# Kernel tuning notes

Hardware: AMD Instinct MI355X
Metric: run time of the kernel (lower is better)

The kernel has to match this reference:

```python
import jax, jax.numpy as jnp
import numpy as np

SIZE = 896      # GRU hidden size
HALF = SIZE // 2
BINS = 256      # 2**(bits/2), bits=16
B, T = 16, 1000


def _scale(t):
    # [0, BINS-1] ints -> [-1, 1] floats
    return t.astype(jnp.float32) / ((BINS - 1) / 2.0) - 1.0


def setup_inputs() -> dict:
    key = jax.random.key(0)
    ks = jax.random.split(key, 13)
    s = 0.05
    return {
        "conditional": jax.random.normal(ks[0], (B, T, 3, SIZE), jnp.float32),
        "gru_input_bias": jax.random.normal(ks[1], (3 * SIZE,), jnp.float32) * s,
        "W_h": jax.random.normal(ks[2], (3 * SIZE, SIZE), jnp.float32) * s,   # project_hidden
        "b_h": jax.random.normal(ks[3], (3 * SIZE,), jnp.float32) * s,
        "W_ci": jax.random.normal(ks[4], (3 * HALF, 2), jnp.float32) * s,     # project_coarse_input
        "b_ci": jax.random.normal(ks[5], (3 * HALF,), jnp.float32) * s,
        "W_fi": jax.random.normal(ks[6], (3 * HALF, 3), jnp.float32) * s,     # project_fine_input
        "b_fi": jax.random.normal(ks[7], (3 * HALF,), jnp.float32) * s,
        "W_bc": jax.random.normal(ks[8], (BINS, HALF), jnp.float32) * s,      # to_bins_coarse
        "b_bc": jax.random.normal(ks[9], (BINS,), jnp.float32) * s,
        "W_bf": jax.random.normal(ks[10], (BINS, HALF), jnp.float32) * s,     # to_bins_fine
        "b_bf": jax.random.normal(ks[11], (BINS,), jnp.float32) * s,
    }


def reference(conditional, gru_input_bias, W_h, b_h, W_ci, b_ci, W_fi, b_fi,
              W_bc, b_bc, W_bf, b_bf):
    # Fold input-GRU biases into the conditional (as the torch code does in-place)
    cond = conditional + gru_input_bias.reshape(3, SIZE)  # [B,T,3,SIZE]
    # split each gate into coarse/fine halves and regroup as (r,u,e)
    cc = jnp.concatenate([cond[:, :, 0, :HALF], cond[:, :, 1, :HALF], cond[:, :, 2, :HALF]], -1)
    cf = jnp.concatenate([cond[:, :, 0, HALF:], cond[:, :, 1, HALF:], cond[:, :, 2, HALF:]], -1)
    cc = jnp.transpose(cc, (1, 0, 2))  # [T,B,3*HALF]
    cf = jnp.transpose(cf, (1, 0, 2))
    sample_key = jax.random.key(1)

    # initial state: split_signal(0) -> coarse=fine=0 -> scaled to -1
    init = (-jnp.ones((B, 1), jnp.float32), -jnp.ones((B, 1), jnp.float32),
            jnp.zeros((B, HALF), jnp.float32), jnp.zeros((B, HALF), jnp.float32))

    def step(carry, xs):
        cv, fv, ch, fh = carry
        ccond, fcond, t = xs
        k1, k2 = jax.random.split(jax.random.fold_in(sample_key, t))
        hidden = jnp.concatenate([ch, fh], 1)                   # [B,SIZE]
        hp = hidden @ W_h.T + b_h                               # [B,3*SIZE]
        hcr, hfr, hcu, hfu, hce, hfe = jnp.split(hp, 6, axis=1)
        h_cru = jnp.concatenate([hcr, hcu], 1)
        h_fru = jnp.concatenate([hfr, hfu], 1)
        # coarse half-step
        cin = jnp.concatenate([cv, fv], 1)                      # [B,2]
        cp = cin @ W_ci.T + b_ci + ccond                        # [B,3*HALF]
        ru = jax.nn.sigmoid(cp[:, :SIZE] + h_cru)
        r, u = jnp.split(ru, 2, axis=1)
        e = jnp.tanh(r * hce + cp[:, SIZE:])
        ch = u * ch + (1.0 - u) * e
        logits_c = ch @ W_bc.T + b_bc                           # [B,BINS]
        sc = jax.random.categorical(k1, jax.nn.log_softmax(logits_c, axis=1))
        cv = _scale(sc)[:, None]
        # fine half-step
        fin = jnp.concatenate([cin, cv], 1)                     # [B,3]
        fp = fin @ W_fi.T + b_fi + fcond
        ru = jax.nn.sigmoid(fp[:, :SIZE] + h_fru)
        r, u = jnp.split(ru, 2, axis=1)
        e = jnp.tanh(r * hfe + fp[:, SIZE:])
        fh = u * fh + (1.0 - u) * e
        logits_f = fh @ W_bf.T + b_bf
        sf = jax.random.categorical(k2, jax.nn.log_softmax(logits_f, axis=1))
        fv = _scale(sf)[:, None]
        return (cv, fv, ch, fh), (sc, sf)

    (cv, fv, ch, fh), (oc, of) = jax.lax.scan(step, init, (cc, cf, jnp.arange(T)))
    hidden = jnp.concatenate([ch, fh], 1)
    return oc.T, of.T, hidden  # [B,T] int, [B,T] int, [B,SIZE]
```

## Files before the change

kernel.cpp:

```cpp
#include <hip/hip_runtime.h>
#include <stdint.h>

#define BB 16
#define TT 1000
#define SZ 896
#define HF 448
#define NC 112
#define NWG 240
#define LDS_FLOATS 30112
#define LDS_BYTES (LDS_FLOATS * 4)

typedef float f32x4 __attribute__((ext_vector_type(4)));
typedef float f32x2 __attribute__((ext_vector_type(2)));

__device__ float g_hid[2 * BB * SZ];
__device__ float g_hpc4[BB * HF * 4];
__device__ float g_hpf4[BB * HF * 4];
__device__ uint32_t g_cdone[NC * 16];
__device__ uint32_t g_chrdy[BB * 16];
__device__ uint32_t g_fhrdy[BB * 16];
__device__ unsigned long long g_afl[BB * 4 * 8];
__device__ unsigned long long g_bfl[BB * 4 * 8];

__device__ __forceinline__ void cload4x4(const float* p, f32x4& a0, f32x4& a1, f32x4& a2, f32x4& a3) {
  asm volatile(
      "global_load_dwordx4 %0, %4, off sc0 sc1\n\t"
      "global_load_dwordx4 %1, %4, off offset:16 sc0 sc1\n\t"
      "global_load_dwordx4 %2, %4, off offset:32 sc0 sc1\n\t"
      "global_load_dwordx4 %3, %4, off offset:48 sc0 sc1\n\t"
      "s_waitcnt vmcnt(0)"
      : "=&v"(a0), "=&v"(a1), "=&v"(a2), "=&v"(a3) : "v"(p) : "memory");
}
__device__ __forceinline__ f32x4 cload1x4(const float* p) {
  f32x4 a;
  asm volatile("global_load_dwordx4 %0, %1, off sc0 sc1\n\ts_waitcnt vmcnt(0)"
               : "=&v"(a) : "v"(p) : "memory");
  return a;
}
__device__ __forceinline__ void cstore4d(float* p, f32x4 v) {
  asm volatile("global_store_dwordx4 %0, %1, off sc0 sc1\n\ts_waitcnt vmcnt(0)"
               :: "v"(p), "v"(v) : "memory");
}
__device__ __forceinline__ void cstore1u_nw(uint32_t* p, uint32_t v) {
  asm volatile("global_store_dword %0, %1, off sc0 sc1" :: "v"(p), "v"(v) : "memory");
}
__device__ __forceinline__ void cstore2u_nw(unsigned long long* p, f32x2 v) {
  asm volatile("global_store_dwordx2 %0, %1, off sc0 sc1" :: "v"(p), "v"(v) : "memory");
}

__device__ __forceinline__ void waitFlag(uint32_t* f, uint32_t target) {
  while (__hip_atomic_load(f, __ATOMIC_RELAXED, __HIP_MEMORY_SCOPE_AGENT) < target)
    __builtin_amdgcn_s_sleep(1);
}
__device__ __forceinline__ void waitFlagA(uint32_t* f, uint32_t target) {
  while (__hip_atomic_load(f, __ATOMIC_RELAXED, __HIP_MEMORY_SCOPE_AGENT) < target)
    __builtin_amdgcn_s_sleep(2);
}
__device__ __forceinline__ unsigned long long waitFlag64(unsigned long long* f, uint32_t tag) {
  unsigned long long u;
  while ((uint32_t)((u = __hip_atomic_load(f, __ATOMIC_RELAXED, __HIP_MEMORY_SCOPE_AGENT)) >> 48) < tag)
    __builtin_amdgcn_s_sleep(1);
  return u;
}

__device__ __forceinline__ uint32_t rotl32(uint32_t v, int d) {
  return (v << d) | (v >> (32 - d));
}

__device__ __forceinline__ uint2 tf2(uint32_t k0, uint32_t k1, uint32_t x0, uint32_t x1) {
  const uint32_t k2 = k0 ^ k1 ^ 0x1BD11BDAu;
  x0 += k0; x1 += k1;
  x0 += x1; x1 = rotl32(x1,13); x1 ^= x0;
  x0 += x1; x1 = rotl32(x1,15); x1 ^= x0;
  x0 += x1; x1 = rotl32(x1,26); x1 ^= x0;
  x0 += x1; x1 = rotl32(x1, 6); x1 ^= x0;
  x0 += k1; x1 += k2 + 1u;
  x0 += x1; x1 = rotl32(x1,17); x1 ^= x0;
  x0 += x1; x1 = rotl32(x1,29); x1 ^= x0;
  x0 += x1; x1 = rotl32(x1,16); x1 ^= x0;
  x0 += x1; x1 = rotl32(x1,24); x1 ^= x0;
  x0 += k2; x1 += k0 + 2u;
  x0 += x1; x1 = rotl32(x1,13); x1 ^= x0;
  x0 += x1; x1 = rotl32(x1,15); x1 ^= x0;
  x0 += x1; x1 = rotl32(x1,26); x1 ^= x0;
  x0 += x1; x1 = rotl32(x1, 6); x1 ^= x0;
  x0 += k0; x1 += k1 + 3u;
  x0 += x1; x1 = rotl32(x1,17); x1 ^= x0;
  x0 += x1; x1 = rotl32(x1,29); x1 ^= x0;
  x0 += x1; x1 = rotl32(x1,16); x1 ^= x0;
  x0 += x1; x1 = rotl32(x1,24); x1 ^= x0;
  x0 += k1; x1 += k2 + 4u;
  x0 += x1; x1 = rotl32(x1,13); x1 ^= x0;
  x0 += x1; x1 = rotl32(x1,15); x1 ^= x0;
  x0 += x1; x1 = rotl32(x1,26); x1 ^= x0;
  x0 += x1; x1 = rotl32(x1, 6); x1 ^= x0;
  x0 += k2; x1 += k0 + 5u;
  return make_uint2(x0, x1);
}

__device__ __forceinline__ float gumbel_bits(uint32_t bits) {
  const float tiny = 1.17549435e-38f;
  float f = __uint_as_float((bits >> 9) | 0x3f800000u) - 1.0f;
  float u = fmaxf(tiny, f + tiny);
  return -logf(-logf(u));
}

__device__ __forceinline__ void logits64(const float* __restrict__ wlds,
                                         const float* __restrict__ vec,
                                         float* __restrict__ plds, int tid) {
  const int w = tid >> 6, lane = tid & 63;
  float a = 0.f;
  const float* wp = wlds + (56 * w) * 65 + lane;
  const float* cp = vec + 56 * w;
#pragma unroll 8
  for (int ii = 0; ii < 56; ++ii)
    a = fmaf(cp[ii], wp[ii * 65], a);
  plds[(w << 6) | lane] = a;
}

__global__ __launch_bounds__(256, 1) void wavernn_init() {
  const int idx = blockIdx.x * 256 + threadIdx.x;
  g_hid[idx] = 0.f;
  if (idx < NC * 16) g_cdone[idx] = 0u;
  if (idx < BB * 16) { g_chrdy[idx] = 0u; g_fhrdy[idx] = 0u; }
  if (idx < BB * 4 * 8) { g_afl[idx] = 0ull; g_bfl[idx] = 0ull; }
}

__global__ __launch_bounds__(512, 1) void wavernn_main(
    const float* __restrict__ cond, const float* __restrict__ gib,
    const float* __restrict__ W_h,  const float* __restrict__ b_h,
    const float* __restrict__ W_ci, const float* __restrict__ b_ci,
    const float* __restrict__ W_fi, const float* __restrict__ b_fi,
    const float* __restrict__ W_bc, const float* __restrict__ b_bc,
    const float* __restrict__ W_bf, const float* __restrict__ b_bf,
    float* __restrict__ out) {
  extern __shared__ float smem[];
  const int wg = blockIdx.x, tid = threadIdx.x;

  if (wg < NC) {
    float* hlds = smem;
    const int wave = tid >> 6, lane = tid & 63;
    const int l32 = lane >> 1, b2 = lane & 1;
    const int tp = wave >> 2;
    const int chan = (wg << 2) | (wave & 3);
    const int rb = tp ? (HF + chan) : chan;
    float4 w[3][7];
    float brow[3];
#pragma unroll
    for (int r = 0; r < 3; ++r) {
      const int row = r * SZ + rb;
      brow[r] = b_h[row];
#pragma unroll
      for (int m = 0; m < 7; ++m)
        w[r][m] = *(const float4*)&W_h[(size_t)row * SZ + 4 * l32 + 128 * m];
    }
    const int r16 = tid & 15, c28 = tid >> 4;

    for (int t = 0; t < TT; ++t) {
      const int p = (t & 1) ^ 1;
      if (tid < BB) waitFlagA(&g_chrdy[tid * 16], (uint32_t)t);
      __syncthreads();
      if (c28 < 28) {
        const float* src = g_hid + (size_t)p * BB * SZ + r16 * SZ + c28 * 16;
        f32x4 a0, a1, a2, a3;
        cload4x4(src, a0, a1, a2, a3);
        float* dst = hlds + r16 * 900 + c28 * 16;
        *(f32x4*)(dst) = a0; *(f32x4*)(dst + 4) = a1;
        *(f32x4*)(dst + 8) = a2; *(f32x4*)(dst + 12) = a3;
      }
      __syncthreads();
      float acc[3][8];
#pragma unroll
      for (int r = 0; r < 3; ++r)
#pragma unroll
        for (int i = 0; i < 8; ++i) acc[r][i] = 0.f;
#pragma unroll
      for (int i = 0; i < 8; ++i) {
        const int b = b2 + 2 * i;
        const float* hb = hlds + b * 900 + 4 * l32;
        const float4 h0 = *(const float4*)(hb);
        const float4 h1 = *(const float4*)(hb + 128);
        const float4 h2 = *(const float4*)(hb + 256);
#pragma unroll
        for (int r = 0; r < 3; ++r) {
          float s = acc[r][i];
          s = fmaf(w[r][0].x, h0.x, s); s = fmaf(w[r][0].y, h0.y, s);
          s = fmaf(w[r][0].z, h0.z, s); s = fmaf(w[r][0].w, h0.w, s);
          s = fmaf(w[r][1].x, h1.x, s); s = fmaf(w[r][1].y, h1.y, s);
          s = fmaf(w[r][1].z, h1.z, s); s = fmaf(w[r][1].w, h1.w, s);
          s = fmaf(w[r][2].x, h2.x, s); s = fmaf(w[r][2].y, h2.y, s);
          s = fmaf(w[r][2].z, h2.z, s); s = fmaf(w[r][2].w, h2.w, s);
          acc[r][i] = s;
        }
        if (l32 < 16) {
          const float4 h3 = *(const float4*)(hb + 384);
#pragma unroll
          for (int r = 0; r < 3; ++r) {
            float s = acc[r][i];
            s = fmaf(w[r][3].x, h3.x, s); s = fmaf(w[r][3].y, h3.y, s);
            s = fmaf(w[r][3].z, h3.z, s); s = fmaf(w[r][3].w, h3.w, s);
            acc[r][i] = s;
          }
        }
      }
      if (tid < BB) waitFlag(&g_fhrdy[tid * 16], (uint32_t)t);
      __syncthreads();
      if (c28 < 28) {
        const float* src = g_hid + (size_t)p * BB * SZ + r16 * SZ + HF + c28 * 16;
        f32x4 a0, a1, a2, a3;
        cload4x4(src, a0, a1, a2, a3);
        float* dst = hlds + r16 * 900 + HF + c28 * 16;
        *(f32x4*)(dst) = a0; *(f32x4*)(dst + 4) = a1;
        *(f32x4*)(dst + 8) = a2; *(f32x4*)(dst + 12) = a3;
      }
      __syncthreads();
#pragma unroll
      for (int i = 0; i < 8; ++i) {
        const int b = b2 + 2 * i;
        const float* hb = hlds + b * 900 + 4 * l32;
        if (l32 >= 16) {
          const float4 h3 = *(const float4*)(hb + 384);
#pragma unroll
          for (int r = 0; r < 3; ++r) {
            float s = acc[r][i];
            s = fmaf(w[r][3].x, h3.x, s); s = fmaf(w[r][3].y, h3.y, s);
            s = fmaf(w[r][3].z, h3.z, s); s = fmaf(w[r][3].w, h3.w, s);
            acc[r][i] = s;
          }
        }
        const float4 h4 = *(const float4*)(hb + 512);
        const float4 h5 = *(const float4*)(hb + 640);
        const float4 h6 = *(const float4*)(hb + 768);
#pragma unroll
        for (int r = 0; r < 3; ++r) {
          float s = acc[r][i];
          s = fmaf(w[r][4].x, h4.x, s); s = fmaf(w[r][4].y, h4.y, s);
          s = fmaf(w[r][4].z, h4.z, s); s = fmaf(w[r][4].w, h4.w, s);
          s = fmaf(w[r][5].x, h5.x, s); s = fmaf(w[r][5].y, h5.y, s);
          s = fmaf(w[r][5].z, h5.z, s); s = fmaf(w[r][5].w, h5.w, s);
          s = fmaf(w[r][6].x, h6.x, s); s = fmaf(w[r][6].y, h6.y, s);
          s = fmaf(w[r][6].z, h6.z, s); s = fmaf(w[r][6].w, h6.w, s);
          acc[r][i] = s;
        }
      }
#pragma unroll
      for (int r = 0; r < 3; ++r)
#pragma unroll
        for (int i = 0; i < 8; ++i) {
          float v = acc[r][i];
          v += __shfl_xor(v, 2);
          v += __shfl_xor(v, 4);
          v += __shfl_xor(v, 8);
          v += __shfl_xor(v, 16);
          v += __shfl_xor(v, 32);
          acc[r][i] = v;
        }
      if (lane < 16) {
        const int bb = lane, i = lane >> 1;
        f32x4 hv;
        hv.x = acc[0][i] + brow[0];
        hv.y = acc[1][i] + brow[1];
        hv.z = acc[2][i] + brow[2];
        hv.w = 0.f;
        float* dst = (tp ? g_hpf4 : g_hpc4) + ((size_t)bb * HF + chan) * 4;
        cstore4d(dst, hv);
      }
      __syncthreads();
      if (tid == 0) cstore1u_nw(&g_cdone[wg * 16], (uint32_t)(t + 1));
    }
  } else {
    const int swg = wg - NC;
    const int b = swg >> 3;
    const int role = (swg >> 2) & 1;
    const int k = swg & 3;
    float* wlds = smem;
    float* vlds = smem + 29120;
    float* plds = smem + 29568;
    float* aS = smem + 30080;
    int*   aI = (int*)(smem + 30084);
    float* bS = smem + 30088;
    int*   bI = (int*)(smem + 30092);
    {
      const float* Wm = role ? W_bf : W_bc;
      for (int i = tid; i < HF * 64; i += 512) {
        const int bn = i / HF, kk = i - bn * HF;
        wlds[kk * 65 + bn] = Wm[(size_t)(64 * k + bn) * HF + kk];
      }
    }
    const float* bias = role ? b_bf : b_bc;
    float gw0[3], gw1[3], gw2[3], gbe[3], pc[3];
    if (tid < HF) {
      if (role == 0) {
#pragma unroll
        for (int g = 0; g < 3; ++g) {
          const int rr = g * HF + tid;
          gw0[g] = W_ci[2 * rr]; gw1[g] = W_ci[2 * rr + 1]; gw2[g] = 0.f;
          gbe[g] = b_ci[rr] + gib[g * SZ + tid];
          pc[g] = cond[(((size_t)b * TT) * 3 + g) * SZ + tid];
        }
      } else {
#pragma unroll
        for (int g = 0; g < 3; ++g) {
          const int rr = g * HF + tid;
          gw0[g] = W_fi[3 * rr]; gw1[g] = W_fi[3 * rr + 1]; gw2[g] = W_fi[3 * rr + 2];
          gbe[g] = b_fi[rr] + gib[g * SZ + HF + tid];
          pc[g] = cond[(((size_t)b * TT) * 3 + g) * SZ + HF + tid];
        }
      }
      vlds[tid] = 0.f;
    }
    __syncthreads();
    float cvO = -1.f;
    float fvO = -1.f;

    for (int t = 0; t < TT; ++t) {
      const int q = t & 1;
      const uint2 kf = tf2(0u, 1u, 0u, (uint32_t)t);
      float gub = 0.f;
      if (tid < 64) {
        const uint2 kk = role ? tf2(kf.x, kf.y, 0u, 1u) : tf2(kf.x, kf.y, 0u, 0u);
        const uint2 o = tf2(kk.x, kk.y, 0u, (uint32_t)(b * 256 + 64 * k + tid));
        gub = gumbel_bits(o.x ^ o.y);
      }
      if (role == 0) {
        if (t > 0 && tid >= 452 && tid < 456) {
          const unsigned long long u = waitFlag64(&g_bfl[(b * 4 + (tid - 452)) * 8], (uint32_t)t);
          bS[tid - 452] = __uint_as_float((uint32_t)u);
          bI[tid - 452] = (int)((u >> 40) & 255u);
        }
        if (tid < NC) waitFlag(&g_cdone[tid * 16], (uint32_t)(t + 1));
        __syncthreads();
        float fvv = -1.f;
        if (t > 0) {
          float ms = bS[0]; int sf = bI[0];
#pragma unroll
          for (int m = 1; m < 4; ++m) {
            const float so = bS[m]; const int io = bI[m];
            if (so > ms || (so == ms && io < sf)) { ms = so; sf = io; }
          }
          fvv = (float)sf / 127.5f - 1.0f;
        }
        if (tid < HF) {
          const f32x4 hp = cload1x4(&g_hpc4[((size_t)b * HF + tid) * 4]);
          const float cp0 = fmaf(cvO, gw0[0], fmaf(fvv, gw1[0], gbe[0])) + pc[0];
          const float cp1 = fmaf(cvO, gw0[1], fmaf(fvv, gw1[1], gbe[1])) + pc[1];
          const float cp2 = fmaf(cvO, gw0[2], fmaf(fvv, gw1[2], gbe[2])) + pc[2];
          const float rg = 1.f / (1.f + expf(-(cp0 + hp.x)));
          const float ug = 1.f / (1.f + expf(-(cp1 + hp.y)));
          const float eg = tanhf(fmaf(rg, hp.z, cp2));
          vlds[tid] = ug * vlds[tid] + (1.f - ug) * eg;
        }
        __syncthreads();
        if (k == 0) {
          if (tid < 112)
            cstore4d(&g_hid[(size_t)q * BB * SZ + b * SZ + 4 * tid], *(f32x4*)&vlds[4 * tid]);
          __syncthreads();
          if (tid == 0) cstore1u_nw(&g_chrdy[b * 16], (uint32_t)(t + 1));
        }
        logits64(wlds, vlds, plds, tid);
        __syncthreads();
        if (tid < 64) {
          const float p0 = plds[tid],       p1 = plds[64 + tid];
          const float p2 = plds[128 + tid], p3 = plds[192 + tid];
          const float p4 = plds[256 + tid], p5 = plds[320 + tid];
          const float p6 = plds[384 + tid], p7 = plds[448 + tid];
          const float sum = ((p0 + p1) + (p2 + p3)) + ((p4 + p5) + (p6 + p7));
          float s = (sum + bias[64 * k + tid]) + gub;
          int idx = 64 * k + tid;
#pragma unroll
          for (int m = 1; m < 64; m <<= 1) {
            const float so = __shfl_xor(s, m);
            const int io = __shfl_xor(idx, m);
            if (so > s || (so == s && io < idx)) { s = so; idx = io; }
          }
          if (tid == 0) {
            f32x2 v; v.x = s;
            v.y = __uint_as_float(((uint32_t)(t + 1) << 16) | ((uint32_t)idx << 8));
            cstore2u_nw(&g_afl[(b * 4 + k) * 8], v);
          }
        }
        if (tid >= 448 && tid < 452) {
          const unsigned long long u = waitFlag64(&g_afl[(b * 4 + (tid - 448)) * 8], (uint32_t)(t + 1));
          aS[tid - 448] = __uint_as_float((uint32_t)u);
          aI[tid - 448] = (int)((u >> 40) & 255u);
        }
        __syncthreads();
        {
          float ms = aS[0]; int sc = aI[0];
#pragma unroll
          for (int m = 1; m < 4; ++m) {
            const float so = aS[m]; const int io = aI[m];
            if (so > ms || (so == ms && io < sc)) { ms = so; sc = io; }
          }
          cvO = (float)sc / 127.5f - 1.0f;
          if (k == 0 && tid == 0) out[b * TT + t] = (float)sc;
        }
        if (tid < HF && t + 1 < TT) {
#pragma unroll
          for (int g = 0; g < 3; ++g)
            pc[g] = cond[(((size_t)b * TT + (t + 1)) * 3 + g) * SZ + tid];
        }
      } else {
        if (tid < NC) waitFlag(&g_cdone[tid * 16], (uint32_t)(t + 1));
        __syncthreads();
        f32x4 hp = {0.f, 0.f, 0.f, 0.f};
        if (tid < HF) hp = cload1x4(&g_hpf4[((size_t)b * HF + tid) * 4]);
        if (tid >= 448 && tid < 452) {
          const unsigned long long u = waitFlag64(&g_afl[(b * 4 + (tid - 448)) * 8], (uint32_t)(t + 1));
          aS[tid - 448] = __uint_as_float((uint32_t)u);
          aI[tid - 448] = (int)((u >> 40) & 255u);
        }
        __syncthreads();
        float ms = aS[0]; int sc = aI[0];
#pragma unroll
        for (int m = 1; m < 4; ++m) {
          const float so = aS[m]; const int io = aI[m];
          if (so > ms || (so == ms && io < sc)) { ms = so; sc = io; }
        }
        const float cvNew = (float)sc / 127.5f - 1.0f;
        if (tid < HF) {
          const float fp0 = fmaf(cvO, gw0[0], fmaf(fvO, gw1[0], fmaf(cvNew, gw2[0], gbe[0]))) + pc[0];
          const float fp1 = fmaf(cvO, gw0[1], fmaf(fvO, gw1[1], fmaf(cvNew, gw2[1], gbe[1]))) + pc[1];
          const float fp2 = fmaf(cvO, gw0[2], fmaf(fvO, gw1[2], fmaf(cvNew, gw2[2], gbe[2]))) + pc[2];
          const float rg = 1.f / (1.f + expf(-(fp0 + hp.x)));
          const float ug = 1.f / (1.f + expf(-(fp1 + hp.y)));
          const float eg = tanhf(fmaf(rg, hp.z, fp2));
          vlds[tid] = ug * vlds[tid] + (1.f - ug) * eg;
        }
        __syncthreads();
        if (k == 0) {
          if (tid < 112)
            cstore4d(&g_hid[(size_t)q * BB * SZ + b * SZ + HF + 4 * tid], *(f32x4*)&vlds[4 * tid]);
          __syncthreads();
          if (tid == 0) cstore1u_nw(&g_fhrdy[b * 16], (uint32_t)(t + 1));
        }
        logits64(wlds, vlds, plds, tid);
        __syncthreads();
        if (tid < 64) {
          const float p0 = plds[tid],       p1 = plds[64 + tid];
          const float p2 = plds[128 + tid], p3 = plds[192 + tid];
          const float p4 = plds[256 + tid], p5 = plds[320 + tid];
          const float p6 = plds[384 + tid], p7 = plds[448 + tid];
          const float sum = ((p0 + p1) + (p2 + p3)) + ((p4 + p5) + (p6 + p7));
          float s = (sum + bias[64 * k + tid]) + gub;
          int idx = 64 * k + tid;
#pragma unroll
          for (int m = 1; m < 64; m <<= 1) {
            const float so = __shfl_xor(s, m);
            const int io = __shfl_xor(idx, m);
            if (so > s || (so == s && io < idx)) { s = so; idx = io; }
          }
          if (tid == 0) {
            f32x2 v; v.x = s;
            v.y = __uint_as_float(((uint32_t)(t + 1) << 16) | ((uint32_t)idx << 8));
            cstore2u_nw(&g_bfl[(b * 4 + k) * 8], v);
          }
        }
        if (tid >= 448 && tid < 452) {
          const unsigned long long u = waitFlag64(&g_bfl[(b * 4 + (tid - 448)) * 8], (uint32_t)(t + 1));
          bS[tid - 448] = __uint_as_float((uint32_t)u);
          bI[tid - 448] = (int)((u >> 40) & 255u);
        }
        __syncthreads();
        {
          float msf = bS[0]; int sf = bI[0];
#pragma unroll
          for (int m = 1; m < 4; ++m) {
            const float so = bS[m]; const int io = bI[m];
            if (so > msf || (so == msf && io < sf)) { msf = so; sf = io; }
          }
          fvO = (float)sf / 127.5f - 1.0f;
          if (k == 0 && tid == 0) out[BB * TT + b * TT + t] = (float)sf;
        }
        cvO = cvNew;
        if (tid < HF && t + 1 < TT) {
#pragma unroll
          for (int g = 0; g < 3; ++g)
            pc[g] = cond[(((size_t)b * TT + (t + 1)) * 3 + g) * SZ + HF + tid];
        }
      }
    }
    if (k == 0 && tid < HF) {
      if (role == 0) out[2 * BB * TT + (size_t)b * SZ + tid] = vlds[tid];
      else           out[2 * BB * TT + (size_t)b * SZ + HF + tid] = vlds[tid];
    }
  }
}

extern "C" void kernel_launch(void* const* d_in, const int* in_sizes, int n_in,
                              void* d_out, int out_size, void* d_ws, size_t ws_size,
                              hipStream_t stream) {
  (void)in_sizes; (void)n_in; (void)out_size; (void)d_ws; (void)ws_size;
  const float* cond = (const float*)d_in[0];
  const float* gib  = (const float*)d_in[1];
  const float* W_h  = (const float*)d_in[2];
  const float* b_h  = (const float*)d_in[3];
  const float* W_ci = (const float*)d_in[4];
  const float* b_ci = (const float*)d_in[5];
  const float* W_fi = (const float*)d_in[6];
  const float* b_fi = (const float*)d_in[7];
  const float* W_bc = (const float*)d_in[8];
  const float* b_bc = (const float*)d_in[9];
  const float* W_bf = (const float*)d_in[10];
  const float* b_bf = (const float*)d_in[11];
  float* out = (float*)d_out;
  hipFuncSetAttribute((const void*)wavernn_main,
                      hipFuncAttributeMaxDynamicSharedMemorySize, LDS_BYTES);
  wavernn_init<<<NC, 256, 0, stream>>>();
  wavernn_main<<<NWG, 512, LDS_BYTES, stream>>>(cond, gib, W_h, b_h, W_ci, b_ci,
                                                W_fi, b_fi, W_bc, b_bc, W_bf, b_bf, out);
}
```

Measured before the change: 13.01 ms.

## Replace separate ready flags with step tags embedded alongside each data value

Each hidden-state and projection value is now stored next to a float timestep tag. Consumers poll the data itself until every tag reaches the expected step, instead of waiting on separate counter flags. This removes the store-wait-barrier-then-flag round trips and the extra flag polls on the inter-workgroup critical path, and every one of the four k-workgroups now publishes its own slice. In exchange the exchanged buffers double in size and the spin loops reload wider data, and it relies on 8-byte pairs being written atomically.

```diff
diff --git a/kernel.cpp b/kernel.cpp
--- a/kernel.cpp
+++ b/kernel.cpp
@@ -13,48 +13,44 @@
 typedef float f32x4 __attribute__((ext_vector_type(4)));
 typedef float f32x2 __attribute__((ext_vector_type(2)));
 
-__device__ float g_hid[2 * BB * SZ];
-__device__ float g_hpc4[BB * HF * 4];
-__device__ float g_hpf4[BB * HF * 4];
-__device__ uint32_t g_cdone[NC * 16];
-__device__ uint32_t g_chrdy[BB * 16];
-__device__ uint32_t g_fhrdy[BB * 16];
+__device__ float g_hc[BB * HF * 2];
+__device__ float g_hf[BB * HF * 2];
+__device__ float g_hpc[BB * HF * 8];
+__device__ float g_hpf[BB * HF * 8];
 __device__ unsigned long long g_afl[BB * 4 * 8];
 __device__ unsigned long long g_bfl[BB * 4 * 8];
 
-__device__ __forceinline__ void cload4x4(const float* p, f32x4& a0, f32x4& a1, f32x4& a2, f32x4& a3) {
+#define au(x) __float_as_uint(x)
+
+__device__ __forceinline__ void cload7x4(const float* p, f32x4& a0, f32x4& a1, f32x4& a2,
+                                         f32x4& a3, f32x4& a4, f32x4& a5, f32x4& a6) {
   asm volatile(
-      "global_load_dwordx4 %0, %4, off sc0 sc1\n\t"
-      "global_load_dwordx4 %1, %4, off offset:16 sc0 sc1\n\t"
-      "global_load_dwordx4 %2, %4, off offset:32 sc0 sc1\n\t"
-      "global_load_dwordx4 %3, %4, off offset:48 sc0 sc1\n\t"
+      "global_load_dwordx4 %0, %7, off sc0 sc1\n\t"
+      "global_load_dwordx4 %1, %7, off offset:16 sc0 sc1\n\t"
+      "global_load_dwordx4 %2, %7, off offset:32 sc0 sc1\n\t"
+      "global_load_dwordx4 %3, %7, off offset:48 sc0 sc1\n\t"
+      "global_load_dwordx4 %4, %7, off offset:64 sc0 sc1\n\t"
+      "global_load_dwordx4 %5, %7, off offset:80 sc0 sc1\n\t"
+      "global_load_dwordx4 %6, %7, off offset:96 sc0 sc1\n\t"
       "s_waitcnt vmcnt(0)"
-      : "=&v"(a0), "=&v"(a1), "=&v"(a2), "=&v"(a3) : "v"(p) : "memory");
-}
-__device__ __forceinline__ f32x4 cload1x4(const float* p) {
-  f32x4 a;
-  asm volatile("global_load_dwordx4 %0, %1, off sc0 sc1\n\ts_waitcnt vmcnt(0)"
-               : "=&v"(a) : "v"(p) : "memory");
-  return a;
-}
-__device__ __forceinline__ void cstore4d(float* p, f32x4 v) {
-  asm volatile("global_store_dwordx4 %0, %1, off sc0 sc1\n\ts_waitcnt vmcnt(0)"
-               :: "v"(p), "v"(v) : "memory");
-}
-__device__ __forceinline__ void cstore1u_nw(uint32_t* p, uint32_t v) {
-  asm volatile("global_store_dword %0, %1, off sc0 sc1" :: "v"(p), "v"(v) : "memory");
+      : "=&v"(a0), "=&v"(a1), "=&v"(a2), "=&v"(a3), "=&v"(a4), "=&v"(a5), "=&v"(a6)
+      : "v"(p) : "memory");
+}
+__device__ __forceinline__ void cload2x4(const float* p, f32x4& a, f32x4& b) {
+  asm volatile(
+      "global_load_dwordx4 %0, %2, off sc0 sc1\n\t"
+      "global_load_dwordx4 %1, %2, off offset:16 sc0 sc1\n\t"
+      "s_waitcnt vmcnt(0)"
+      : "=&v"(a), "=&v"(b) : "v"(p) : "memory");
+}
+__device__ __forceinline__ void cstore4f_nw(float* p, f32x4 v) {
+  asm volatile("global_store_dwordx4 %0, %1, off sc0 sc1" :: "v"(p), "v"(v) : "memory");
+}
+__device__ __forceinline__ void cstore2f_nw(float* p, f32x2 v) {
+  asm volatile("global_store_dwordx2 %0, %1, off sc0 sc1" :: "v"(p), "v"(v) : "memory");
 }
 __device__ __forceinline__ void cstore2u_nw(unsigned long long* p, f32x2 v) {
   asm volatile("global_store_dwordx2 %0, %1, off sc0 sc1" :: "v"(p), "v"(v) : "memory");
-}
-
-__device__ __forceinline__ void waitFlag(uint32_t* f, uint32_t target) {
-  while (__hip_atomic_load(f, __ATOMIC_RELAXED, __HIP_MEMORY_SCOPE_AGENT) < target)
-    __builtin_amdgcn_s_sleep(1);
-}
-__device__ __forceinline__ void waitFlagA(uint32_t* f, uint32_t target) {
-  while (__hip_atomic_load(f, __ATOMIC_RELAXED, __HIP_MEMORY_SCOPE_AGENT) < target)
-    __builtin_amdgcn_s_sleep(2);
 }
 __device__ __forceinline__ unsigned long long waitFlag64(unsigned long long* f, uint32_t tag) {
   unsigned long long u;
@@ -118,11 +114,11 @@
   plds[(w << 6) | lane] = a;
 }
 
-__global__ __launch_bounds__(256, 1) void wavernn_init() {
-  const int idx = blockIdx.x * 256 + threadIdx.x;
-  g_hid[idx] = 0.f;
-  if (idx < NC * 16) g_cdone[idx] = 0u;
-  if (idx < BB * 16) { g_chrdy[idx] = 0u; g_fhrdy[idx] = 0u; }
+__global__ __launch_bounds__(512, 1) void wavernn_init() {
+  const int idx = blockIdx.x * 512 + threadIdx.x;
+  g_hpc[idx] = 0.f;
+  g_hpf[idx] = 0.f;
+  if (idx < BB * HF * 2) { g_hc[idx] = 0.f; g_hf[idx] = 0.f; }
   if (idx < BB * 4 * 8) { g_afl[idx] = 0ull; g_bfl[idx] = 0ull; }
 }
 
@@ -154,20 +150,28 @@
       for (int m = 0; m < 7; ++m)
         w[r][m] = *(const float4*)&W_h[(size_t)row * SZ + 4 * l32 + 128 * m];
     }
-    const int r16 = tid & 15, c28 = tid >> 4;
+    const int bat = tid >> 5, chk = tid & 31;
+    const float* srcC = g_hc + ((size_t)bat * HF + chk * 14) * 2;
+    const float* srcF = g_hf + ((size_t)bat * HF + chk * 14) * 2;
+    float* dstC = hlds + bat * 900 + chk * 14;
+    float* dstF = dstC + HF;
 
     for (int t = 0; t < TT; ++t) {
-      const int p = (t & 1) ^ 1;
-      if (tid < BB) waitFlagA(&g_chrdy[tid * 16], (uint32_t)t);
+      const uint32_t tgh = au((float)t);
+      f32x4 a0, a1, a2, a3, a4, a5, a6;
+      for (;;) {
+        cload7x4(srcC, a0, a1, a2, a3, a4, a5, a6);
+        if (au(a0.y) >= tgh && au(a0.w) >= tgh && au(a1.y) >= tgh && au(a1.w) >= tgh &&
+            au(a2.y) >= tgh && au(a2.w) >= tgh && au(a3.y) >= tgh && au(a3.w) >= tgh &&
+            au(a4.y) >= tgh && au(a4.w) >= tgh && au(a5.y) >= tgh && au(a5.w) >= tgh &&
+            au(a6.y) >= tgh && au(a6.w) >= tgh) break;
+        __builtin_amdgcn_s_sleep(1);
+      }
       __syncthreads();
-      if (c28 < 28) {
-        const float* src = g_hid + (size_t)p * BB * SZ + r16 * SZ + c28 * 16;
-        f32x4 a0, a1, a2, a3;
-        cload4x4(src, a0, a1, a2, a3);
-        float* dst = hlds + r16 * 900 + c28 * 16;
-        *(f32x4*)(dst) = a0; *(f32x4*)(dst + 4) = a1;
-        *(f32x4*)(dst + 8) = a2; *(f32x4*)(dst + 12) = a3;
-      }
+      dstC[0] = a0.x; dstC[1] = a0.z; dstC[2] = a1.x; dstC[3] = a1.z;
+      dstC[4] = a2.x; dstC[5] = a2.z; dstC[6] = a3.x; dstC[7] = a3.z;
+      dstC[8] = a4.x; dstC[9] = a4.z; dstC[10] = a5.x; dstC[11] = a5.z;
+      dstC[12] = a6.x; dstC[13] = a6.z;
       __syncthreads();
       float acc[3][8];
 #pragma unroll
@@ -203,16 +207,18 @@
           }
         }
       }
-      if (tid < BB) waitFlag(&g_fhrdy[tid * 16], (uint32_t)t);
-      __syncthreads();
-      if (c28 < 28) {
-        const float* src = g_hid + (size_t)p * BB * SZ + r16 * SZ + HF + c28 * 16;
-        f32x4 a0, a1, a2, a3;
-        cload4x4(src, a0, a1, a2, a3);
-        float* dst = hlds + r16 * 900 + HF + c28 * 16;
-        *(f32x4*)(dst) = a0; *(f32x4*)(dst + 4) = a1;
-        *(f32x4*)(dst + 8) = a2; *(f32x4*)(dst + 12) = a3;
-      }
+      for (;;) {
+        cload7x4(srcF, a0, a1, a2, a3, a4, a5, a6);
+        if (au(a0.y) >= tgh && au(a0.w) >= tgh && au(a1.y) >= tgh && au(a1.w) >= tgh &&
+            au(a2.y) >= tgh && au(a2.w) >= tgh && au(a3.y) >= tgh && au(a3.w) >= tgh &&
+            au(a4.y) >= tgh && au(a4.w) >= tgh && au(a5.y) >= tgh && au(a5.w) >= tgh &&
+            au(a6.y) >= tgh && au(a6.w) >= tgh) break;
+        __builtin_amdgcn_s_sleep(1);
+      }
+      dstF[0] = a0.x; dstF[1] = a0.z; dstF[2] = a1.x; dstF[3] = a1.z;
+      dstF[4] = a2.x; dstF[5] = a2.z; dstF[6] = a3.x; dstF[7] = a3.z;
+      dstF[8] = a4.x; dstF[9] = a4.z; dstF[10] = a5.x; dstF[11] = a5.z;
+      dstF[12] = a6.x; dstF[13] = a6.z;
       __syncthreads();
 #pragma unroll
       for (int i = 0; i < 8; ++i) {
@@ -257,16 +263,13 @@
         }
       if (lane < 16) {
         const int bb = lane, i = lane >> 1;
-        f32x4 hv;
-        hv.x = acc[0][i] + brow[0];
-        hv.y = acc[1][i] + brow[1];
-        hv.z = acc[2][i] + brow[2];
-        hv.w = 0.f;
-        float* dst = (tp ? g_hpf4 : g_hpc4) + ((size_t)bb * HF + chan) * 4;
-        cstore4d(dst, hv);
-      }
-      __syncthreads();
-      if (tid == 0) cstore1u_nw(&g_cdone[wg * 16], (uint32_t)(t + 1));
+        const float tgf = (float)(t + 1);
+        f32x4 q; q.x = acc[0][i] + brow[0]; q.y = tgf; q.z = acc[1][i] + brow[1]; q.w = tgf;
+        f32x2 r2; r2.x = acc[2][i] + brow[2]; r2.y = tgf;
+        float* dst = (tp ? g_hpf : g_hpc) + ((size_t)bb * HF + chan) * 8;
+        cstore4f_nw(dst, q);
+        cstore2f_nw(dst + 4, r2);
+      }
     }
   } else {
     const int swg = wg - NC;
@@ -310,11 +313,10 @@
       vlds[tid] = 0.f;
     }
     __syncthreads();
-    float cvO = -1.f;
-    float fvO = -1.f;
+    float cvO = -1.f, fvO = -1.f;
+    const float* hpSrc = (role ? g_hpf : g_hpc) + ((size_t)b * HF + (tid < HF ? tid : 0)) * 8;
 
     for (int t = 0; t < TT; ++t) {
-      const int q = t & 1;
       const uint2 kf = tf2(0u, 1u, 0u, (uint32_t)t);
       float gub = 0.f;
       if (tid < 64) {
@@ -322,13 +324,21 @@
         const uint2 o = tf2(kk.x, kk.y, 0u, (uint32_t)(b * 256 + 64 * k + tid));
         gub = gumbel_bits(o.x ^ o.y);
       }
+      const uint32_t tgp = au((float)(t + 1));
+      f32x4 h0, h1;
+      if (tid < HF) {
+        for (;;) {
+          cload2x4(hpSrc, h0, h1);
+          if (au(h0.y) >= tgp && au(h0.w) >= tgp && au(h1.y) >= tgp) break;
+          __builtin_amdgcn_s_sleep(1);
+        }
+      }
       if (role == 0) {
         if (t > 0 && tid >= 452 && tid < 456) {
           const unsigned long long u = waitFlag64(&g_bfl[(b * 4 + (tid - 452)) * 8], (uint32_t)t);
           bS[tid - 452] = __uint_as_float((uint32_t)u);
           bI[tid - 452] = (int)((u >> 40) & 255u);
         }
-        if (tid < NC) waitFlag(&g_cdone[tid * 16], (uint32_t)(t + 1));
         __syncthreads();
         float fvv = -1.f;
         if (t > 0) {
@@ -341,21 +351,19 @@
           fvv = (float)sf / 127.5f - 1.0f;
         }
         if (tid < HF) {
-          const f32x4 hp = cload1x4(&g_hpc4[((size_t)b * HF + tid) * 4]);
           const float cp0 = fmaf(cvO, gw0[0], fmaf(fvv, gw1[0], gbe[0])) + pc[0];
           const float cp1 = fmaf(cvO, gw0[1], fmaf(fvv, gw1[1], gbe[1])) + pc[1];
           const float cp2 = fmaf(cvO, gw0[2], fmaf(fvv, gw1[2], gbe[2])) + pc[2];
-          const float rg = 1.f / (1.f + expf(-(cp0 + hp.x)));
-          const float ug = 1.f / (1.f + expf(-(cp1 + hp.y)));
-          const float eg = tanhf(fmaf(rg, hp.z, cp2));
+          const float rg = 1.f / (1.f + expf(-(cp0 + h0.x)));
+          const float ug = 1.f / (1.f + expf(-(cp1 + h0.z)));
+          const float eg = tanhf(fmaf(rg, h1.x, cp2));
           vlds[tid] = ug * vlds[tid] + (1.f - ug) * eg;
         }
         __syncthreads();
-        if (k == 0) {
-          if (tid < 112)
-            cstore4d(&g_hid[(size_t)q * BB * SZ + b * SZ + 4 * tid], *(f32x4*)&vlds[4 * tid]);
-          __syncthreads();
-          if (tid == 0) cstore1u_nw(&g_chrdy[b * 16], (uint32_t)(t + 1));
+        if (tid < 112) {
+          const int pos = 112 * k + tid;
+          f32x2 pv; pv.x = vlds[pos]; pv.y = (float)(t + 1);
+          cstore2f_nw(g_hc + ((size_t)b * HF + pos) * 2, pv);
         }
         logits64(wlds, vlds, plds, tid);
         __syncthreads();
@@ -401,10 +409,6 @@
             pc[g] = cond[(((size_t)b * TT + (t + 1)) * 3 + g) * SZ + tid];
         }
       } else {
-        if (tid < NC) waitFlag(&g_cdone[tid * 16], (uint32_t)(t + 1));
-        __syncthreads();
-        f32x4 hp = {0.f, 0.f, 0.f, 0.f};
-        if (tid < HF) hp = cload1x4(&g_hpf4[((size_t)b * HF + tid) * 4]);
         if (tid >= 448 && tid < 452) {
           const unsigned long long u = waitFlag64(&g_afl[(b * 4 + (tid - 448)) * 8], (uint32_t)(t + 1));
           aS[tid - 448] = __uint_as_float((uint32_t)u);
@@ -422,17 +426,16 @@
           const float fp0 = fmaf(cvO, gw0[0], fmaf(fvO, gw1[0], fmaf(cvNew, gw2[0], gbe[0]))) + pc[0];
           const float fp1 = fmaf(cvO, gw0[1], fmaf(fvO, gw1[1], fmaf(cvNew, gw2[1], gbe[1]))) + pc[1];
           const float fp2 = fmaf(cvO, gw0[2], fmaf(fvO, gw1[2], fmaf(cvNew, gw2[2], gbe[2]))) + pc[2];
-          const float rg = 1.f / (1.f + expf(-(fp0 + hp.x)));
-          const float ug = 1.f / (1.f + expf(-(fp1 + hp.y)));
-          const float eg = tanhf(fmaf(rg, hp.z, fp2));
+          const float rg = 1.f / (1.f + expf(-(fp0 + h0.x)));
+          const float ug = 1.f / (1.f + expf(-(fp1 + h0.z)));
+          const float eg = tanhf(fmaf(rg, h1.x, fp2));
           vlds[tid] = ug * vlds[tid] + (1.f - ug) * eg;
         }
         __syncthreads();
-        if (k == 0) {
-          if (tid < 112)
-            cstore4d(&g_hid[(size_t)q * BB * SZ + b * SZ + HF + 4 * tid], *(f32x4*)&vlds[4 * tid]);
-          __syncthreads();
-          if (tid == 0) cstore1u_nw(&g_fhrdy[b * 16], (uint32_t)(t + 1));
+        if (tid < 112) {
+          const int pos = 112 * k + tid;
+          f32x2 pv; pv.x = vlds[pos]; pv.y = (float)(t + 1);
+          cstore2f_nw(g_hf + ((size_t)b * HF + pos) * 2, pv);
         }
         logits64(wlds, vlds, plds, tid);
         __syncthreads();
@@ -506,7 +509,7 @@
   float* out = (float*)d_out;
   hipFuncSetAttribute((const void*)wavernn_main,
                       hipFuncAttributeMaxDynamicSharedMemorySize, LDS_BYTES);
-  wavernn_init<<<NC, 256, 0, stream>>>();
+  wavernn_init<<<NC, 512, 0, stream>>>();
   wavernn_main<<<NWG, 512, LDS_BYTES, stream>>>(cond, gib, W_h, b_h, W_ci, b_ci,
                                                 W_fi, b_fi, W_bc, b_bc, W_bf, b_bf, out);
 }
```

New measurement: 20.30 ms. +56.0%, slower.
